# Optimization experiments

Hardware: AMD Instinct MI355X
Metric: run time of the kernel (lower is better)

## Reference

```python
import jax, jax.numpy as jnp
import numpy as np

D_CONV = 4
D_STATE = 16
DT_RANK = 64


def _silu(x):
    return x * jax.nn.sigmoid(x)


def setup_inputs() -> dict:
    key = jax.random.key(0)
    ks = jax.random.split(key, 10)
    B, L, dim = 2, 1024, 1024
    d_inner = 2 * dim
    s = lambda fan: 1.0 / np.sqrt(fan)
    inp = {
        "x": jax.random.normal(ks[0], (B, L, dim), jnp.float32),
        "ln_w": jnp.ones((dim,), jnp.float32),
        "ln_b": jnp.zeros((dim,), jnp.float32),
        "w_in": jax.random.normal(ks[1], (2 * d_inner, dim), jnp.float32) * s(dim),
        "conv_w": jax.random.normal(ks[2], (d_inner, D_CONV), jnp.float32) * s(D_CONV),
        "conv_b": jnp.zeros((d_inner,), jnp.float32),
        "w_xproj": jax.random.normal(ks[3], (DT_RANK + 2 * D_STATE, d_inner), jnp.float32) * s(d_inner),
        "w_dt": jax.random.normal(ks[4], (d_inner, DT_RANK), jnp.float32) * s(DT_RANK),
        "b_dt": jax.random.normal(ks[5], (d_inner,), jnp.float32) * 0.1,
        # S4D-real init: A = -(1..d_state) per channel
        "a_log": jnp.tile(jnp.log(jnp.arange(1, D_STATE + 1, dtype=jnp.float32)), (d_inner, 1)),
        "d_skip": jnp.ones((d_inner,), jnp.float32),
        "w_out": jax.random.normal(ks[6], (dim, d_inner), jnp.float32) * s(d_inner),
    }
    return inp


def reference(x, ln_w, ln_b, w_in, conv_w, conv_b, w_xproj, w_dt, b_dt, a_log, d_skip, w_out):
    B, L, dim = x.shape
    residual = x

    # LayerNorm
    mu = jnp.mean(x, axis=-1, keepdims=True)
    var = jnp.mean((x - mu) ** 2, axis=-1, keepdims=True)
    xn = (x - mu) * jax.lax.rsqrt(var + 1e-5) * ln_w + ln_b

    # in_proj -> (x_ssm, z) each (B, L, d_inner)
    xz = jnp.einsum("bld,ed->ble", xn, w_in)
    d_inner = xz.shape[-1] // 2
    xs, z = xz[..., :d_inner], xz[..., d_inner:]

    # depthwise causal conv1d (kernel D_CONV) + SiLU
    xp = jnp.pad(xs, ((0, 0), (D_CONV - 1, 0), (0, 0)))
    xc = conv_b
    for k in range(D_CONV):
        xc = xc + conv_w[:, k] * xp[:, k : k + L, :]
    u = _silu(xc)  # (B, L, d_inner)

    # x_proj -> dt, B, C
    x_dbl = jnp.einsum("ble,re->blr", u, w_xproj)
    dt_r = x_dbl[..., :DT_RANK]
    B_ssm = x_dbl[..., DT_RANK : DT_RANK + D_STATE]         # (B, L, n)
    C_ssm = x_dbl[..., DT_RANK + D_STATE :]                 # (B, L, n)

    dt = jax.nn.softplus(jnp.einsum("blr,er->ble", dt_r, w_dt) + b_dt)  # (B, L, d_inner)

    A = -jnp.exp(a_log)  # (d_inner, n)
    deltaA = jnp.exp(jnp.einsum("ble,en->blen", dt, A))            # (B, L, e, n)
    deltaBu = jnp.einsum("ble,bln,ble->blen", dt, B_ssm, u)        # (B, L, e, n)

    # selective scan over L
    def step(h, ins):
        dA_t, dBu_t, C_t = ins
        h = dA_t * h + dBu_t                       # (B, e, n)
        y = jnp.einsum("ben,bn->be", h, C_t)
        return h, y

    h0 = jnp.zeros((B, d_inner, D_STATE), xs.dtype)
    _, ys = jax.lax.scan(
        step,
        h0,
        (deltaA.transpose(1, 0, 2, 3), deltaBu.transpose(1, 0, 2, 3), C_ssm.transpose(1, 0, 2)),
    )
    y = ys.transpose(1, 0, 2) + u * d_skip         # (B, L, e)

    y = y * _silu(z)
    out = jnp.einsum("ble,de->bld", y, w_out)
    return residual + out
```

## Files before the change

kernel.cpp:

```cpp
#include <hip/hip_runtime.h>
#include <hip/hip_bf16.h>


#define LC 32
#define NCHUNK 32

typedef short bf16x8 __attribute__((ext_vector_type(8)));
typedef float f32x4  __attribute__((ext_vector_type(4)));

static __device__ __forceinline__ float siluf(float x) { return x / (1.f + __expf(-x)); }
static __device__ __forceinline__ unsigned short f2bf(float f) {
    unsigned int u = __float_as_uint(f);
    unsigned int r = (u + 0x7fffu + ((u >> 16) & 1u)) >> 16;
    return (unsigned short)r;
}
static __device__ __forceinline__ float bfb(unsigned short u) {
    return __uint_as_float(((unsigned int)u) << 16);
}
static __device__ __forceinline__ void gload_lds16(const void* g, void* l) {
    __builtin_amdgcn_global_load_lds(
        (const __attribute__((address_space(1))) void*)g,
        (__attribute__((address_space(3))) void*)l, 16, 0, 0);
}

__global__ __launch_bounds__(256) void setup_kernel(
    const float* __restrict__ w_in,  unsigned short* __restrict__ w_in_b,
    const float* __restrict__ w_out, unsigned short* __restrict__ w_out_b,
    const float* __restrict__ w_dt,  unsigned short* __restrict__ w_dt_b,
    const float* __restrict__ x,
    const float* __restrict__ ln_w,
    const float* __restrict__ ln_b,
    unsigned short* __restrict__ xn)
{
    int bid = blockIdx.x, tid = threadIdx.x;
    if (bid < 6272) {
        int i = bid * 256 + tid;
        const float* in; unsigned short* outp; int j;
        if (i < 1048576)      { in = w_in;  outp = w_in_b;  j = i; }
        else if (i < 1572864) { in = w_out; outp = w_out_b; j = i - 1048576; }
        else if (i < 1605632) { in = w_dt;  outp = w_dt_b;  j = i - 1572864; }
        else return;
        float4 v = reinterpret_cast<const float4*>(in)[j];
        ushort4 o = { f2bf(v.x), f2bf(v.y), f2bf(v.z), f2bf(v.w) };
        reinterpret_cast<ushort4*>(outp)[j] = o;
        return;
    }
    int m = bid - 6272;
    const float4* xr = reinterpret_cast<const float4*>(x) + (size_t)m * 256;
    float4 r = xr[tid];
    float f0 = r.x, f1 = r.y, f2 = r.z, f3 = r.w;
    float s  = f0 + f1 + f2 + f3;
    float s2 = f0*f0 + f1*f1 + f2*f2 + f3*f3;
    #pragma unroll
    for (int off = 32; off > 0; off >>= 1) {
        s  += __shfl_down(s, off);
        s2 += __shfl_down(s2, off);
    }
    __shared__ float red[8];
    if ((tid & 63) == 0) { red[tid >> 6] = s; red[4 + (tid >> 6)] = s2; }
    __syncthreads();
    float st = red[0] + red[1] + red[2] + red[3];
    float qt = red[4] + red[5] + red[6] + red[7];
    float mu   = st * (1.f / 1024.f);
    float var  = qt * (1.f / 1024.f) - mu * mu;
    float rstd = rsqrtf(var + 1e-5f);
    float4 wv = reinterpret_cast<const float4*>(ln_w)[tid];
    float4 bv = reinterpret_cast<const float4*>(ln_b)[tid];
    ushort4 o = { f2bf((f0 - mu) * rstd * wv.x + bv.x),
                  f2bf((f1 - mu) * rstd * wv.y + bv.y),
                  f2bf((f2 - mu) * rstd * wv.z + bv.z),
                  f2bf((f3 - mu) * rstd * wv.w + bv.w) };
    reinterpret_cast<ushort4*>(xn + (size_t)m * 1024)[tid] = o;
}

__global__ __launch_bounds__(256) void gemm_bf16_nt(
    const unsigned short* __restrict__ A, int lda,
    const unsigned short* __restrict__ B, int ldb,
    int Kslice,
    float* __restrict__ C, unsigned short* __restrict__ Cb, int ldc,
    const float* __restrict__ bias,
    int ep, size_t Cstride)
{
    __shared__ short As[3 * 64 * 32];
    __shared__ short Bs[3 * 128 * 32];
    int tid = threadIdx.x;
    int z = blockIdx.z;
    A += (size_t)z * Kslice;
    B += (size_t)z * Kslice;
    C += (size_t)z * Cstride;

    int gx = gridDim.x;
    int wg = blockIdx.y * gx + blockIdx.x;
    int nwg = gx * gridDim.y;
    int cpx = nwg >> 3;
    int swz = (wg & 7) * cpx + (wg >> 3);
    int bx = swz % gx, by = swz / gx;

    int m0 = by * 64, n0 = bx * 128;
    int lane = tid & 63, wave = tid >> 6;
    int wm = (wave >> 1) * 32, wn = (wave & 1) * 64;
    int frow = lane & 15, fq = lane >> 4;

    f32x4 acc[2][4] = {};

    int lrow = lane >> 2;
    int scol = (lane & 3) * 8;
    const unsigned short* AgL = A + (size_t)(m0 + wave * 16 + lrow) * lda + scol;
    const unsigned short* BgL = B + (size_t)(n0 + wave * 16 + lrow) * ldb + scol;
    int aoff = (wave * 16) * 32;
    int boff = (wave * 16) * 32;

    #pragma unroll
    for (int p = 0; p < 2; ++p) {
        int nk = p * 32;
        gload_lds16(AgL + nk,                    As + p * 2048 + aoff);
        gload_lds16(BgL + nk,                    Bs + p * 4096 + boff);
        gload_lds16(BgL + (size_t)64 * ldb + nk, Bs + p * 4096 + boff + 64 * 32);
    }

    int cur = 0;
    for (int k0 = 0; k0 < Kslice; k0 += 32) {
        if (k0 + 32 < Kslice) {
            asm volatile("s_waitcnt vmcnt(3) lgkmcnt(0)" ::: "memory");
        } else {
            asm volatile("s_waitcnt vmcnt(0) lgkmcnt(0)" ::: "memory");
        }
        __builtin_amdgcn_s_barrier();
        int nk = k0 + 64;
        if (nk < Kslice) {
            int stg = cur - 1; if (stg < 0) stg = 2;
            gload_lds16(AgL + nk,                    As + stg * 2048 + aoff);
            gload_lds16(BgL + nk,                    Bs + stg * 4096 + boff);
            gload_lds16(BgL + (size_t)64 * ldb + nk, Bs + stg * 4096 + boff + 64 * 32);
        }
        const short* Ac = As + cur * 2048;
        const short* Bc = Bs + cur * 4096;
        bf16x8 af[2], bfr[4];
        #pragma unroll
        for (int i = 0; i < 2; ++i)
            af[i] = *reinterpret_cast<const bf16x8*>(Ac + (wm + i * 16 + frow) * 32 + fq * 8);
        #pragma unroll
        for (int j = 0; j < 4; ++j)
            bfr[j] = *reinterpret_cast<const bf16x8*>(Bc + (wn + j * 16 + frow) * 32 + fq * 8);
        #pragma unroll
        for (int i = 0; i < 2; ++i)
            #pragma unroll
            for (int j = 0; j < 4; ++j)
                acc[i][j] = __builtin_amdgcn_mfma_f32_16x16x32_bf16(af[i], bfr[j], acc[i][j], 0, 0, 0);
        cur = (cur == 2) ? 0 : cur + 1;
    }

    int cn = lane & 15, rq = (lane >> 4) * 4;
    #pragma unroll
    for (int i = 0; i < 2; ++i) {
        #pragma unroll
        for (int j = 0; j < 4; ++j) {
            #pragma unroll
            for (int r = 0; r < 4; ++r) {
                int row = m0 + wm + i * 16 + rq + r;
                int col = n0 + wn + j * 16 + cn;
                float v = acc[i][j][r];
                if (ep == 0) {
                    C[(size_t)row * ldc + col] = v;
                } else if (ep == 1) {
                    v += bias[col];
                    v = (v > 20.f) ? v : log1pf(__expf(v));
                    Cb[(size_t)row * ldc + col] = f2bf(v);
                } else {
                    Cb[(size_t)row * ldc + col] = f2bf(v);
                }
            }
        }
    }
}

__global__ __launch_bounds__(256) void out_reduce(
    const float* __restrict__ part, const float* __restrict__ x,
    float* __restrict__ out)
{
    int i = blockIdx.x * 256 + threadIdx.x;
    float4 s = reinterpret_cast<const float4*>(x)[i];
    #pragma unroll
    for (int z = 0; z < 4; ++z) {
        float4 p = reinterpret_cast<const float4*>(part + (size_t)z * 2097152)[i];
        s.x += p.x; s.y += p.y; s.z += p.z; s.w += p.w;
    }
    reinterpret_cast<float4*>(out)[i] = s;
}

__global__ __launch_bounds__(256) void xproj_splitk(
    const unsigned short* __restrict__ xz,
    const float* __restrict__ cw,
    const float* __restrict__ cb,
    const float* __restrict__ B,
    unsigned short* __restrict__ u,
    float* __restrict__ part)
{
    __shared__ float As[16][68];
    __shared__ float Bs[16][100];
    int tid = threadIdx.x;
    int m0 = blockIdx.x * 64;
    int k0 = blockIdx.y * 128;
    int tx = tid & 15;
    int ty = tid >> 4;
    float acc[4][6] = {};
    int arow = tid >> 2, akg = (tid & 3) << 2;
    int brow1 = (256 + tid) >> 2, bkg1 = ((256 + tid) & 3) << 2;
    int m = m0 + arow;
    int l = m & 1023;

    for (int ks = 0; ks < 128; ks += 16) {
        int e0 = k0 + ks + akg;
        float xv[4][4];
        #pragma unroll
        for (int kk = 0; kk < 4; ++kk) {
            ushort4 t = make_ushort4(0, 0, 0, 0);
            if (l - 3 + kk >= 0)
                t = *reinterpret_cast<const ushort4*>(xz + (size_t)(m - 3 + kk) * 4096 + e0);
            xv[kk][0] = bfb(t.x); xv[kk][1] = bfb(t.y);
            xv[kk][2] = bfb(t.z); xv[kk][3] = bfb(t.w);
        }
        float4 cbv = *reinterpret_cast<const float4*>(cb + e0);
        float cbs[4] = { cbv.x, cbv.y, cbv.z, cbv.w };
        float res[4];
        #pragma unroll
        for (int j = 0; j < 4; ++j) {
            float4 w = *reinterpret_cast<const float4*>(cw + (size_t)(e0 + j) * 4);
            float a = cbs[j];
            a = fmaf(w.x, xv[0][j], a);
            a = fmaf(w.y, xv[1][j], a);
            a = fmaf(w.z, xv[2][j], a);
            a = fmaf(w.w, xv[3][j], a);
            res[j] = siluf(a);
        }
        ushort4 uo = { f2bf(res[0]), f2bf(res[1]), f2bf(res[2]), f2bf(res[3]) };
        *reinterpret_cast<ushort4*>(u + (size_t)m * 2048 + e0) = uo;

        float4 bv0 = make_float4(0.f, 0.f, 0.f, 0.f), bv1 = bv0;
        if (arow < 96)  bv0 = *reinterpret_cast<const float4*>(B + (size_t)arow * 2048 + k0 + ks + akg);
        if (brow1 < 96) bv1 = *reinterpret_cast<const float4*>(B + (size_t)brow1 * 2048 + k0 + ks + bkg1);
        __syncthreads();
        As[akg + 0][arow] = res[0]; As[akg + 1][arow] = res[1];
        As[akg + 2][arow] = res[2]; As[akg + 3][arow] = res[3];
        if (arow < 96) {
            Bs[akg + 0][arow] = bv0.x; Bs[akg + 1][arow] = bv0.y;
            Bs[akg + 2][arow] = bv0.z; Bs[akg + 3][arow] = bv0.w;
        }
        if (brow1 < 96) {
            Bs[bkg1 + 0][brow1] = bv1.x; Bs[bkg1 + 1][brow1] = bv1.y;
            Bs[bkg1 + 2][brow1] = bv1.z; Bs[bkg1 + 3][brow1] = bv1.w;
        }
        __syncthreads();
        #pragma unroll
        for (int k = 0; k < 16; ++k) {
            float aa[4], bb[6];
            #pragma unroll
            for (int i = 0; i < 4; ++i) aa[i] = As[k][ty * 4 + i];
            #pragma unroll
            for (int j = 0; j < 6; ++j) bb[j] = Bs[k][tx * 6 + j];
            #pragma unroll
            for (int i = 0; i < 4; ++i)
                #pragma unroll
                for (int j = 0; j < 6; ++j)
                    acc[i][j] = fmaf(aa[i], bb[j], acc[i][j]);
        }
    }
    float* p = part + (size_t)blockIdx.y * 196608;
    #pragma unroll
    for (int i = 0; i < 4; ++i)
        #pragma unroll
        for (int j = 0; j < 6; ++j)
            p[(size_t)(m0 + ty * 4 + i) * 96 + tx * 6 + j] = acc[i][j];
}

__global__ __launch_bounds__(256) void xproj_reduce(
    const float* __restrict__ part, float* __restrict__ xdbl,
    unsigned short* __restrict__ dtr)
{
    int i = blockIdx.x * 256 + threadIdx.x;
    float s = 0.f;
    #pragma unroll
    for (int sd = 0; sd < 16; ++sd) s += part[(size_t)sd * 196608 + i];
    xdbl[i] = s;
    int m = i / 96, col = i - m * 96;
    if (col < 64) dtr[(size_t)m * 64 + col] = f2bf(s);
}

__global__ __launch_bounds__(256) void scan_part1(
    const unsigned short* __restrict__ dt,
    const unsigned short* __restrict__ u,
    const float* __restrict__ xdbl,
    const float* __restrict__ a_log,
    float* __restrict__ hpart,
    float* __restrict__ Aprod)
{
    int tid = threadIdx.x;
    int ch = tid >> 2, ng = tid & 3;
    int bid = blockIdx.x;
    int c = bid & 31, et = (bid >> 5) & 31, b = bid >> 10;
    int e = et * 64 + ch;
    float4 al = *reinterpret_cast<const float4*>(a_log + e * 16 + ng * 4);
    float A0 = -__expf(al.x), A1 = -__expf(al.y), A2 = -__expf(al.z), A3 = -__expf(al.w);
    size_t rbase = (size_t)b * 1024 + c * LC;
    const unsigned short* dt_p = dt + rbase * 2048 + e;
    const unsigned short* u_p  = u  + rbase * 2048 + e;
    const float* b_p  = xdbl + rbase * 96 + 64 + ng * 4;
    float h0 = 0.f, h1 = 0.f, h2 = 0.f, h3 = 0.f;
    float P0 = 1.f, P1 = 1.f, P2 = 1.f, P3 = 1.f;
    float dt_c = bfb(dt_p[0]);
    float u_c  = bfb(u_p[0]);
    float4 B_c = *reinterpret_cast<const float4*>(b_p);
    #pragma unroll 8
    for (int l = 0; l < LC; ++l) {
        float dt_n = bfb(dt_p[(size_t)(l + 1) * 2048]);
        float u_n  = bfb(u_p[(size_t)(l + 1) * 2048]);
        float4 B_n = *reinterpret_cast<const float4*>(b_p + (size_t)(l + 1) * 96);
        float du = dt_c * u_c;
        float d0 = __expf(dt_c * A0), d1 = __expf(dt_c * A1);
        float d2 = __expf(dt_c * A2), d3 = __expf(dt_c * A3);
        h0 = fmaf(d0, h0, du * B_c.x); P0 *= d0;
        h1 = fmaf(d1, h1, du * B_c.y); P1 *= d1;
        h2 = fmaf(d2, h2, du * B_c.z); P2 *= d2;
        h3 = fmaf(d3, h3, du * B_c.w); P3 *= d3;
        dt_c = dt_n; u_c = u_n; B_c = B_n;
    }
    size_t oidx = (size_t)c * 65536 + ((size_t)b * 2048 + e) * 16 + ng * 4;
    *reinterpret_cast<float4*>(hpart + oidx) = make_float4(h0, h1, h2, h3);
    *reinterpret_cast<float4*>(Aprod + oidx) = make_float4(P0, P1, P2, P3);
}

__global__ __launch_bounds__(256) void scan_combine(
    const float* __restrict__ hpart,
    const float* __restrict__ Aprod,
    float* __restrict__ hinit)
{
    int t = blockIdx.x * 256 + threadIdx.x;
    float h = 0.f;
    #pragma unroll 8
    for (int c = 0; c < NCHUNK; ++c) {
        hinit[(size_t)c * 65536 + t] = h;
        float P  = Aprod[(size_t)c * 65536 + t];
        float hp = hpart[(size_t)c * 65536 + t];
        h = fmaf(P, h, hp);
    }
}

__global__ __launch_bounds__(256) void scan_part2(
    const unsigned short* __restrict__ dt,
    const unsigned short* __restrict__ u,
    const float* __restrict__ xdbl,
    const unsigned short* __restrict__ xz,
    const float* __restrict__ a_log,
    const float* __restrict__ d_skip,
    const float* __restrict__ hinit,
    unsigned short* __restrict__ y)
{
    int tid = threadIdx.x;
    int ch = tid >> 2, ng = tid & 3;
    int bid = blockIdx.x;
    int c = bid & 31, et = (bid >> 5) & 31, b = bid >> 10;
    int e = et * 64 + ch;
    float4 al = *reinterpret_cast<const float4*>(a_log + e * 16 + ng * 4);
    float A0 = -__expf(al.x), A1 = -__expf(al.y), A2 = -__expf(al.z), A3 = -__expf(al.w);
    float dsk = d_skip[e];
    size_t rbase = (size_t)b * 1024 + c * LC;
    const unsigned short* dt_p = dt + rbase * 2048 + e;
    const unsigned short* u_p  = u  + rbase * 2048 + e;
    const unsigned short* z_p  = xz + rbase * 4096 + 2048 + e;
    const float* bc_p = xdbl + rbase * 96 + 64 + ng * 4;
    unsigned short* y_p = y + rbase * 2048 + e;
    size_t oidx = (size_t)c * 65536 + ((size_t)b * 2048 + e) * 16 + ng * 4;
    float4 hi = *reinterpret_cast<const float4*>(hinit + oidx);
    float h0 = hi.x, h1 = hi.y, h2 = hi.z, h3 = hi.w;
    float dt_c = bfb(dt_p[0]);
    float u_c  = bfb(u_p[0]);
    float4 B_c = *reinterpret_cast<const float4*>(bc_p);
    float4 C_c = *reinterpret_cast<const float4*>(bc_p + 16);
    #pragma unroll 8
    for (int l = 0; l < LC; ++l) {
        float dt_n = bfb(dt_p[(size_t)(l + 1) * 2048]);
        float u_n  = bfb(u_p[(size_t)(l + 1) * 2048]);
        float4 B_n = *reinterpret_cast<const float4*>(bc_p + (size_t)(l + 1) * 96);
        float4 C_n = *reinterpret_cast<const float4*>(bc_p + (size_t)(l + 1) * 96 + 16);
        float du = dt_c * u_c;
        float d0 = __expf(dt_c * A0), d1 = __expf(dt_c * A1);
        float d2 = __expf(dt_c * A2), d3 = __expf(dt_c * A3);
        h0 = fmaf(d0, h0, du * B_c.x);
        h1 = fmaf(d1, h1, du * B_c.y);
        h2 = fmaf(d2, h2, du * B_c.z);
        h3 = fmaf(d3, h3, du * B_c.w);
        float p = h0 * C_c.x + h1 * C_c.y + h2 * C_c.z + h3 * C_c.w;
        p += __shfl_xor(p, 1);
        p += __shfl_xor(p, 2);
        if (ng == 0) {
            float zv = bfb(z_p[(size_t)l * 4096]);
            y_p[(size_t)l * 2048] = f2bf((p + u_c * dsk) * siluf(zv));
        }
        dt_c = dt_n; u_c = u_n; B_c = B_n; C_c = C_n;
    }
}

extern "C" void kernel_launch(void* const* d_in, const int* in_sizes, int n_in,
                              void* d_out, int out_size, void* d_ws, size_t ws_size,
                              hipStream_t stream) {
    const float* x       = (const float*)d_in[0];
    const float* ln_w    = (const float*)d_in[1];
    const float* ln_b    = (const float*)d_in[2];
    const float* w_in    = (const float*)d_in[3];
    const float* conv_w  = (const float*)d_in[4];
    const float* conv_b  = (const float*)d_in[5];
    const float* w_xproj = (const float*)d_in[6];
    const float* w_dt    = (const float*)d_in[7];
    const float* b_dt    = (const float*)d_in[8];
    const float* a_log   = (const float*)d_in[9];
    const float* d_skip  = (const float*)d_in[10];
    const float* w_out   = (const float*)d_in[11];
    float* out = (float*)d_out;

    float* ws = (float*)d_ws;
    unsigned short* xn_b    = (unsigned short*)(ws);
    unsigned short* xz_b    = (unsigned short*)(ws + 1048576);
    unsigned short* u_b     = (unsigned short*)(ws + 5242880);
    float* xdbl  = ws + 7340032;
    unsigned short* dt_b    = (unsigned short*)(ws + 7536640);
    float* hpart = ws + 9633792;
    float* Aprod = ws + 13828096;
    float* hinit = ws + 18022400;
    unsigned short* y_b     = (unsigned short*)(ws + 22216704);
    unsigned short* w_in_b  = (unsigned short*)(ws + 24313856);
    unsigned short* w_out_b = (unsigned short*)(ws + 26411008);
    unsigned short* w_dt_b  = (unsigned short*)(ws + 27459584);
    unsigned short* dtr_b   = (unsigned short*)(ws + 27525120);
    float* xpart = ws + 9633792;
    float* opart = ws + 1048576;

    setup_kernel<<<8320, 256, 0, stream>>>(w_in, w_in_b, w_out, w_out_b, w_dt, w_dt_b,
                                           x, ln_w, ln_b, xn_b);
    gemm_bf16_nt<<<dim3(32, 32, 1), 256, 0, stream>>>(xn_b, 1024, w_in_b, 1024, 1024,
                                                      nullptr, xz_b, 4096, nullptr, 3, 0);
    xproj_splitk<<<dim3(32, 16), 256, 0, stream>>>(xz_b, conv_w, conv_b, w_xproj,
                                                   u_b, xpart);
    xproj_reduce<<<768, 256, 0, stream>>>(xpart, xdbl, dtr_b);
    gemm_bf16_nt<<<dim3(16, 32, 1), 256, 0, stream>>>(dtr_b, 64, w_dt_b, 64, 64,
                                                      nullptr, dt_b, 2048, b_dt, 1, 0);
    scan_part1<<<2048, 256, 0, stream>>>(dt_b, u_b, xdbl, a_log, hpart, Aprod);
    scan_combine<<<256, 256, 0, stream>>>(hpart, Aprod, hinit);
    scan_part2<<<2048, 256, 0, stream>>>(dt_b, u_b, xdbl, xz_b, a_log, d_skip, hinit, y_b);
    gemm_bf16_nt<<<dim3(8, 32, 4), 256, 0, stream>>>(y_b, 2048, w_out_b, 2048, 512,
                                                     opart, nullptr, 1024, nullptr, 0, 2097152);
    out_reduce<<<2048, 256, 0, stream>>>(opart, x, out);
}
```

Measured before the change: 267.3 us.

## Fuse dt projection into scan kernels and use atomic split-K for x_proj

Removes the separate x_proj reduce kernel by accumulating split-K partials directly into xdbl with atomicAdd, after zeroing it in the setup kernel. Also removes the dt GEMM and its bf16 dt buffer: each scan block now computes its 32x64 dt tile with MFMA from xdbl and w_dt, applies bias and softplus, and keeps it in LDS. This cuts two launches and the round trip of a 2x1024x2048 dt tensor through memory. In exchange the dt tile is computed twice (once per scan pass), atomics make the xdbl sum order nondeterministic, and the scan kernels gain a barrier and LDS use.

```diff
diff --git a/kernel.cpp b/kernel.cpp
--- a/kernel.cpp
+++ b/kernel.cpp
@@ -30,7 +30,8 @@
     const float* __restrict__ x,
     const float* __restrict__ ln_w,
     const float* __restrict__ ln_b,
-    unsigned short* __restrict__ xn)
+    unsigned short* __restrict__ xn,
+    float* __restrict__ xdbl)
 {
     int bid = blockIdx.x, tid = threadIdx.x;
     if (bid < 6272) {
@@ -43,6 +44,11 @@
         float4 v = reinterpret_cast<const float4*>(in)[j];
         ushort4 o = { f2bf(v.x), f2bf(v.y), f2bf(v.z), f2bf(v.w) };
         reinterpret_cast<ushort4*>(outp)[j] = o;
+        return;
+    }
+    if (bid >= 8320) {
+        int j = (bid - 8320) * 256 + tid;
+        reinterpret_cast<float4*>(xdbl)[j] = make_float4(0.f, 0.f, 0.f, 0.f);
         return;
     }
     int m = bid - 6272;
@@ -78,7 +84,6 @@
     const unsigned short* __restrict__ B, int ldb,
     int Kslice,
     float* __restrict__ C, unsigned short* __restrict__ Cb, int ldc,
-    const float* __restrict__ bias,
     int ep, size_t Cstride)
 {
     __shared__ short As[3 * 64 * 32];
@@ -162,10 +167,6 @@
                 float v = acc[i][j][r];
                 if (ep == 0) {
                     C[(size_t)row * ldc + col] = v;
-                } else if (ep == 1) {
-                    v += bias[col];
-                    v = (v > 20.f) ? v : log1pf(__expf(v));
-                    Cb[(size_t)row * ldc + col] = f2bf(v);
                 } else {
                     Cb[(size_t)row * ldc + col] = f2bf(v);
                 }
@@ -194,7 +195,7 @@
     const float* __restrict__ cb,
     const float* __restrict__ B,
     unsigned short* __restrict__ u,
-    float* __restrict__ part)
+    float* __restrict__ xdbl)
 {
     __shared__ float As[16][68];
     __shared__ float Bs[16][100];
@@ -265,64 +266,99 @@
                     acc[i][j] = fmaf(aa[i], bb[j], acc[i][j]);
         }
     }
-    float* p = part + (size_t)blockIdx.y * 196608;
     #pragma unroll
     for (int i = 0; i < 4; ++i)
         #pragma unroll
         for (int j = 0; j < 6; ++j)
-            p[(size_t)(m0 + ty * 4 + i) * 96 + tx * 6 + j] = acc[i][j];
-}
-
-__global__ __launch_bounds__(256) void xproj_reduce(
-    const float* __restrict__ part, float* __restrict__ xdbl,
-    unsigned short* __restrict__ dtr)
-{
-    int i = blockIdx.x * 256 + threadIdx.x;
-    float s = 0.f;
-    #pragma unroll
-    for (int sd = 0; sd < 16; ++sd) s += part[(size_t)sd * 196608 + i];
-    xdbl[i] = s;
-    int m = i / 96, col = i - m * 96;
-    if (col < 64) dtr[(size_t)m * 64 + col] = f2bf(s);
+            atomicAdd(&xdbl[(size_t)(m0 + ty * 4 + i) * 96 + tx * 6 + j], acc[i][j]);
+}
+
+static __device__ __forceinline__ void dt_tile(
+    const float* __restrict__ xdbl, const unsigned short* __restrict__ w_dt_b,
+    const float* __restrict__ b_dt, size_t rbase, int et,
+    int lane, int wave, float dtl[LC][64])
+{
+    int frow = lane & 15, fq = lane >> 4;
+    bf16x8 af[2][2], bfr[2];
+    #pragma unroll
+    for (int i = 0; i < 2; ++i)
+        #pragma unroll
+        for (int kk = 0; kk < 2; ++kk) {
+            const float* ap = xdbl + (rbase + i * 16 + frow) * 96 + kk * 32 + fq * 8;
+            float4 a0 = *reinterpret_cast<const float4*>(ap);
+            float4 a1 = *reinterpret_cast<const float4*>(ap + 4);
+            bf16x8 t;
+            t[0] = (short)f2bf(a0.x); t[1] = (short)f2bf(a0.y);
+            t[2] = (short)f2bf(a0.z); t[3] = (short)f2bf(a0.w);
+            t[4] = (short)f2bf(a1.x); t[5] = (short)f2bf(a1.y);
+            t[6] = (short)f2bf(a1.z); t[7] = (short)f2bf(a1.w);
+            af[i][kk] = t;
+        }
+    #pragma unroll
+    for (int kk = 0; kk < 2; ++kk)
+        bfr[kk] = *reinterpret_cast<const bf16x8*>(
+            w_dt_b + (size_t)(et * 64 + wave * 16 + frow) * 64 + kk * 32 + fq * 8);
+    f32x4 dacc[2] = {};
+    #pragma unroll
+    for (int i = 0; i < 2; ++i)
+        #pragma unroll
+        for (int kk = 0; kk < 2; ++kk)
+            dacc[i] = __builtin_amdgcn_mfma_f32_16x16x32_bf16(af[i][kk], bfr[kk], dacc[i], 0, 0, 0);
+    int cn = lane & 15, rq = (lane >> 4) * 4;
+    #pragma unroll
+    for (int i = 0; i < 2; ++i)
+        #pragma unroll
+        for (int r = 0; r < 4; ++r) {
+            int row = i * 16 + rq + r;
+            int col = wave * 16 + cn;
+            float v = dacc[i][r] + b_dt[et * 64 + col];
+            v = (v > 20.f) ? v : log1pf(__expf(v));
+            dtl[row][col] = bfb(f2bf(v));
+        }
 }
 
 __global__ __launch_bounds__(256) void scan_part1(
-    const unsigned short* __restrict__ dt,
     const unsigned short* __restrict__ u,
     const float* __restrict__ xdbl,
+    const unsigned short* __restrict__ w_dt_b,
+    const float* __restrict__ b_dt,
     const float* __restrict__ a_log,
     float* __restrict__ hpart,
     float* __restrict__ Aprod)
 {
+    __shared__ float dtl[LC][64];
     int tid = threadIdx.x;
     int ch = tid >> 2, ng = tid & 3;
+    int lane = tid & 63, wave = tid >> 6;
     int bid = blockIdx.x;
     int c = bid & 31, et = (bid >> 5) & 31, b = bid >> 10;
     int e = et * 64 + ch;
+    size_t rbase = (size_t)b * 1024 + c * LC;
+
+    dt_tile(xdbl, w_dt_b, b_dt, rbase, et, lane, wave, dtl);
+
     float4 al = *reinterpret_cast<const float4*>(a_log + e * 16 + ng * 4);
     float A0 = -__expf(al.x), A1 = -__expf(al.y), A2 = -__expf(al.z), A3 = -__expf(al.w);
-    size_t rbase = (size_t)b * 1024 + c * LC;
-    const unsigned short* dt_p = dt + rbase * 2048 + e;
     const unsigned short* u_p  = u  + rbase * 2048 + e;
     const float* b_p  = xdbl + rbase * 96 + 64 + ng * 4;
     float h0 = 0.f, h1 = 0.f, h2 = 0.f, h3 = 0.f;
     float P0 = 1.f, P1 = 1.f, P2 = 1.f, P3 = 1.f;
-    float dt_c = bfb(dt_p[0]);
     float u_c  = bfb(u_p[0]);
     float4 B_c = *reinterpret_cast<const float4*>(b_p);
+    __syncthreads();
     #pragma unroll 8
     for (int l = 0; l < LC; ++l) {
-        float dt_n = bfb(dt_p[(size_t)(l + 1) * 2048]);
         float u_n  = bfb(u_p[(size_t)(l + 1) * 2048]);
         float4 B_n = *reinterpret_cast<const float4*>(b_p + (size_t)(l + 1) * 96);
-        float du = dt_c * u_c;
-        float d0 = __expf(dt_c * A0), d1 = __expf(dt_c * A1);
-        float d2 = __expf(dt_c * A2), d3 = __expf(dt_c * A3);
+        float dtv = dtl[l][ch];
+        float du = dtv * u_c;
+        float d0 = __expf(dtv * A0), d1 = __expf(dtv * A1);
+        float d2 = __expf(dtv * A2), d3 = __expf(dtv * A3);
         h0 = fmaf(d0, h0, du * B_c.x); P0 *= d0;
         h1 = fmaf(d1, h1, du * B_c.y); P1 *= d1;
         h2 = fmaf(d2, h2, du * B_c.z); P2 *= d2;
         h3 = fmaf(d3, h3, du * B_c.w); P3 *= d3;
-        dt_c = dt_n; u_c = u_n; B_c = B_n;
+        u_c = u_n; B_c = B_n;
     }
     size_t oidx = (size_t)c * 65536 + ((size_t)b * 2048 + e) * 16 + ng * 4;
     *reinterpret_cast<float4*>(hpart + oidx) = make_float4(h0, h1, h2, h3);
@@ -346,25 +382,30 @@
 }
 
 __global__ __launch_bounds__(256) void scan_part2(
-    const unsigned short* __restrict__ dt,
     const unsigned short* __restrict__ u,
     const float* __restrict__ xdbl,
+    const unsigned short* __restrict__ w_dt_b,
+    const float* __restrict__ b_dt,
     const unsigned short* __restrict__ xz,
     const float* __restrict__ a_log,
     const float* __restrict__ d_skip,
     const float* __restrict__ hinit,
     unsigned short* __restrict__ y)
 {
+    __shared__ float dtl[LC][64];
     int tid = threadIdx.x;
     int ch = tid >> 2, ng = tid & 3;
+    int lane = tid & 63, wave = tid >> 6;
     int bid = blockIdx.x;
     int c = bid & 31, et = (bid >> 5) & 31, b = bid >> 10;
     int e = et * 64 + ch;
+    size_t rbase = (size_t)b * 1024 + c * LC;
+
+    dt_tile(xdbl, w_dt_b, b_dt, rbase, et, lane, wave, dtl);
+
     float4 al = *reinterpret_cast<const float4*>(a_log + e * 16 + ng * 4);
     float A0 = -__expf(al.x), A1 = -__expf(al.y), A2 = -__expf(al.z), A3 = -__expf(al.w);
     float dsk = d_skip[e];
-    size_t rbase = (size_t)b * 1024 + c * LC;
-    const unsigned short* dt_p = dt + rbase * 2048 + e;
     const unsigned short* u_p  = u  + rbase * 2048 + e;
     const unsigned short* z_p  = xz + rbase * 4096 + 2048 + e;
     const float* bc_p = xdbl + rbase * 96 + 64 + ng * 4;
@@ -372,19 +413,19 @@
     size_t oidx = (size_t)c * 65536 + ((size_t)b * 2048 + e) * 16 + ng * 4;
     float4 hi = *reinterpret_cast<const float4*>(hinit + oidx);
     float h0 = hi.x, h1 = hi.y, h2 = hi.z, h3 = hi.w;
-    float dt_c = bfb(dt_p[0]);
     float u_c  = bfb(u_p[0]);
     float4 B_c = *reinterpret_cast<const float4*>(bc_p);
     float4 C_c = *reinterpret_cast<const float4*>(bc_p + 16);
+    __syncthreads();
     #pragma unroll 8
     for (int l = 0; l < LC; ++l) {
-        float dt_n = bfb(dt_p[(size_t)(l + 1) * 2048]);
         float u_n  = bfb(u_p[(size_t)(l + 1) * 2048]);
         float4 B_n = *reinterpret_cast<const float4*>(bc_p + (size_t)(l + 1) * 96);
         float4 C_n = *reinterpret_cast<const float4*>(bc_p + (size_t)(l + 1) * 96 + 16);
-        float du = dt_c * u_c;
-        float d0 = __expf(dt_c * A0), d1 = __expf(dt_c * A1);
-        float d2 = __expf(dt_c * A2), d3 = __expf(dt_c * A3);
+        float dtv = dtl[l][ch];
+        float du = dtv * u_c;
+        float d0 = __expf(dtv * A0), d1 = __expf(dtv * A1);
+        float d2 = __expf(dtv * A2), d3 = __expf(dtv * A3);
         h0 = fmaf(d0, h0, du * B_c.x);
         h1 = fmaf(d1, h1, du * B_c.y);
         h2 = fmaf(d2, h2, du * B_c.z);
@@ -396,7 +437,7 @@
             float zv = bfb(z_p[(size_t)l * 4096]);
             y_p[(size_t)l * 2048] = f2bf((p + u_c * dsk) * siluf(zv));
         }
-        dt_c = dt_n; u_c = u_n; B_c = B_n; C_c = C_n;
+        u_c = u_n; B_c = B_n; C_c = C_n;
     }
 }
 
@@ -422,7 +463,6 @@
     unsigned short* xz_b    = (unsigned short*)(ws + 1048576);
     unsigned short* u_b     = (unsigned short*)(ws + 5242880);
     float* xdbl  = ws + 7340032;
-    unsigned short* dt_b    = (unsigned short*)(ws + 7536640);
     float* hpart = ws + 9633792;
     float* Aprod = ws + 13828096;
     float* hinit = ws + 18022400;
@@ -430,23 +470,19 @@
     unsigned short* w_in_b  = (unsigned short*)(ws + 24313856);
     unsigned short* w_out_b = (unsigned short*)(ws + 26411008);
     unsigned short* w_dt_b  = (unsigned short*)(ws + 27459584);
-    unsigned short* dtr_b   = (unsigned short*)(ws + 27525120);
-    float* xpart = ws + 9633792;
     float* opart = ws + 1048576;
 
-    setup_kernel<<<8320, 256, 0, stream>>>(w_in, w_in_b, w_out, w_out_b, w_dt, w_dt_b,
-                                           x, ln_w, ln_b, xn_b);
+    setup_kernel<<<8512, 256, 0, stream>>>(w_in, w_in_b, w_out, w_out_b, w_dt, w_dt_b,
+                                           x, ln_w, ln_b, xn_b, xdbl);
     gemm_bf16_nt<<<dim3(32, 32, 1), 256, 0, stream>>>(xn_b, 1024, w_in_b, 1024, 1024,
-                                                      nullptr, xz_b, 4096, nullptr, 3, 0);
+                                                      nullptr, xz_b, 4096, 3, 0);
     xproj_splitk<<<dim3(32, 16), 256, 0, stream>>>(xz_b, conv_w, conv_b, w_xproj,
-                                                   u_b, xpart);
-    xproj_reduce<<<768, 256, 0, stream>>>(xpart, xdbl, dtr_b);
-    gemm_bf16_nt<<<dim3(16, 32, 1), 256, 0, stream>>>(dtr_b, 64, w_dt_b, 64, 64,
-                                                      nullptr, dt_b, 2048, b_dt, 1, 0);
-    scan_part1<<<2048, 256, 0, stream>>>(dt_b, u_b, xdbl, a_log, hpart, Aprod);
+                                                   u_b, xdbl);
+    scan_part1<<<2048, 256, 0, stream>>>(u_b, xdbl, w_dt_b, b_dt, a_log, hpart, Aprod);
     scan_combine<<<256, 256, 0, stream>>>(hpart, Aprod, hinit);
-    scan_part2<<<2048, 256, 0, stream>>>(dt_b, u_b, xdbl, xz_b, a_log, d_skip, hinit, y_b);
+    scan_part2<<<2048, 256, 0, stream>>>(u_b, xdbl, w_dt_b, b_dt, xz_b, a_log,
+                                         d_skip, hinit, y_b);
     gemm_bf16_nt<<<dim3(8, 32, 4), 256, 0, stream>>>(y_b, 2048, w_out_b, 2048, 512,
-                                                     opart, nullptr, 1024, nullptr, 0, 2097152);
+                                                     opart, nullptr, 1024, 0, 2097152);
     out_reduce<<<2048, 256, 0, stream>>>(opart, x, out);
 }
```

Result: slower. 324.1 us (+21.3%).
